# Optimization experiments

Hardware: AMD Instinct MI355X
Metric: run time of the kernel (lower is better)

The kernel has to match this reference:

```python
import jax, jax.numpy as jnp
import numpy as np

N, E, IN_DIM, H, D = 50000, 1600000, 128, 8, 16


def setup_inputs() -> dict:
    key = jax.random.key(0)
    ks = jax.random.split(key, 9)
    s = 1.0 / np.sqrt(IN_DIM)
    return {
        "h": jax.random.normal(ks[0], (N, IN_DIM), dtype=jnp.float32),
        "Wq": jax.random.normal(ks[1], (IN_DIM, H * D), dtype=jnp.float32) * s,
        "bq": jax.random.normal(ks[2], (H * D,), dtype=jnp.float32) * 0.01,
        "Wk": jax.random.normal(ks[3], (IN_DIM, H * D), dtype=jnp.float32) * s,
        "bk": jax.random.normal(ks[4], (H * D,), dtype=jnp.float32) * 0.01,
        "Wv": jax.random.normal(ks[5], (IN_DIM, H * D), dtype=jnp.float32) * s,
        "bv": jax.random.normal(ks[6], (H * D,), dtype=jnp.float32) * 0.01,
        "src": jax.random.randint(ks[7], (E,), 0, N, dtype=jnp.int32),
        "dst": jax.random.randint(ks[8], (E,), 0, N, dtype=jnp.int32),
    }


def reference(h, Wq, bq, Wk, bk, Wv, bv, src, dst):
    n = h.shape[0]
    # node-level projections, reshaped to [N, H, D]
    Q = (h @ Wq + bq).reshape(n, H, D)
    K = (h @ Wk + bk).reshape(n, H, D)
    V = (h @ Wv + bv).reshape(n, H, D)
    # per-edge score: dot(K[src], Q[dst]) / sqrt(D), exp-clamped -> [E, H]
    score = jnp.sum(K[src] * Q[dst], axis=-1) / np.sqrt(D)
    score = jnp.exp(jnp.clip(score, -5.0, 5.0))
    # score-weighted messages scattered into destination nodes
    m = V[src] * score[:, :, None]                    # [E, H, D]
    wV = jax.ops.segment_sum(m, dst, num_segments=n)  # [N, H, D]
    z = jax.ops.segment_sum(score, dst, num_segments=n)  # [N, H]
    h_out = wV / (z[:, :, None] + 1e-6)
    return h_out.reshape(n, H * D)
```

## Files before the change

### kernel.cpp

```cpp
#include <hip/hip_runtime.h>
#include <hip/hip_bf16.h>

#define IN_DIM 128
#define HH 8
#define DD 16
#define HD 128
#define SCAN_B 256
#define CHUNK 8192

#define MT  64
#define KP  136
#define NCH 128

typedef float f32x4 __attribute__((ext_vector_type(4)));
typedef short s16x8 __attribute__((ext_vector_type(8)));

__device__ __forceinline__ int sniff_fp32(const unsigned short* h_raw) {
  int sane = 0;
#pragma unroll
  for (int i = 0; i < 128; i += 2) {
    const unsigned short u = h_raw[i];
    const int expo = (u >> 7) & 0xFF;
    if (expo >= 112 && expo <= 143) sane++;
  }
  return (sane >= 40) ? 0 : 1;
}

__global__ __launch_bounds__(128) void wt_kernel(
    const unsigned short* __restrict__ h_raw,
    const void* __restrict__ Wq, const void* __restrict__ Wk,
    const void* __restrict__ Wv, __hip_bfloat16* __restrict__ Wt,
    int* __restrict__ flag, int* __restrict__ bucket_size) {
  const int isf = sniff_fp32(h_raw);
  const int n = blockIdx.x;
  const int k = threadIdx.x;
  if (n == 0) {
    if (k == 0) *flag = isf;
    for (int j = k; j < 258; j += 128) bucket_size[j] = 0;
  }
  const int mat = n >> 7;
  const int col = n & 127;
  const void* W = (mat == 0) ? Wq : (mat == 1) ? Wk : Wv;
  float v;
  if (isf) v = ((const float*)W)[(size_t)k * HD + col];
  else     v = __bfloat162float(((const __hip_bfloat16*)W)[(size_t)k * HD + col]);
  Wt[(size_t)n * KP + k] = __float2bfloat16(v);
}

__global__ __launch_bounds__(256) void proj_hist_kernel(
    const void* __restrict__ h, const __hip_bfloat16* __restrict__ Wt,
    const void* __restrict__ bq, const void* __restrict__ bk,
    const void* __restrict__ bv,
    float* __restrict__ Qf, __hip_bfloat16* __restrict__ Kb,
    __hip_bfloat16* __restrict__ Vb,
    const int* __restrict__ flag, int n_nodes,
    const int* __restrict__ dst, int* __restrict__ bucket_size, int n_edges,
    int pgrid) {
  __shared__ short Bs[NCH * KP];
  __shared__ short As[MT * KP];

  const int tid = threadIdx.x;

  if (blockIdx.x >= pgrid) {
    int* lh = (int*)Bs;
    const int e0 = (blockIdx.x - pgrid) * CHUNK;
    const int e1 = (e0 + CHUNK < n_edges) ? e0 + CHUNK : n_edges;
    lh[tid] = 0;
    __syncthreads();
    for (int e = e0 + tid; e < e1; e += 256) atomicAdd(&lh[dst[e] >> 8], 1);
    __syncthreads();
    if (lh[tid] > 0) atomicAdd(&bucket_size[tid], lh[tid]);
    return;
  }

  const int node0 = blockIdx.x * MT;
  const int isf = *flag;

#pragma unroll
  for (int j = 0; j < 16; ++j) {
    const int pid = tid + j * 256;
    const int m = pid >> 6;
    const int kk = (pid & 63) * 2;
    const int g = node0 + m;
    unsigned int pack = 0;
    if (g < n_nodes) {
      if (isf) {
        const float2 f2 = *(const float2*)((const float*)h + (size_t)g * HD + kk);
        const __hip_bfloat16 b0 = __float2bfloat16(f2.x);
        const __hip_bfloat16 b1 = __float2bfloat16(f2.y);
        pack = (unsigned int)(*(const unsigned short*)&b0) |
               ((unsigned int)(*(const unsigned short*)&b1) << 16);
      } else {
        pack = *(const unsigned int*)((const __hip_bfloat16*)h +
                                      (size_t)g * HD + kk);
      }
    }
    *(unsigned int*)&As[m * KP + kk] = pack;
  }
  __syncthreads();

  const int wave = tid >> 6;
  const int lane = tid & 63;
  const int l15 = lane & 15;
  const int quad = lane >> 4;

  s16x8 afrag[4];
#pragma unroll
  for (int k4 = 0; k4 < 4; ++k4)
    afrag[k4] = *(const s16x8*)&As[(wave * 16 + l15) * KP + k4 * 32 + quad * 8];

  for (int c = 0; c < 3; ++c) {
    __syncthreads();
    const uint4* gsrc = (const uint4*)(Wt + (size_t)c * NCH * KP);
    for (int j = tid; j < (NCH * KP * 2) / 16; j += 256)
      ((uint4*)Bs)[j] = gsrc[j];
    __syncthreads();

    f32x4 acc[8];
#pragma unroll
    for (int t = 0; t < 8; ++t) acc[t] = (f32x4){0.f, 0.f, 0.f, 0.f};

#pragma unroll
    for (int t = 0; t < 8; ++t) {
#pragma unroll
      for (int k4 = 0; k4 < 4; ++k4) {
        const s16x8 bfrag =
            *(const s16x8*)&Bs[(t * 16 + l15) * KP + k4 * 32 + quad * 8];
        acc[t] = __builtin_amdgcn_mfma_f32_16x16x32_bf16(afrag[k4], bfrag,
                                                         acc[t], 0, 0, 0);
      }
    }

    const void* bp = (c == 0) ? bq : (c == 1) ? bk : bv;
#pragma unroll
    for (int t = 0; t < 8; ++t) {
      const int ncol = t * 16 + l15;
      const float bias = isf ? ((const float*)bp)[ncol]
                             : __bfloat162float(((const __hip_bfloat16*)bp)[ncol]);
#pragma unroll
      for (int r = 0; r < 4; ++r) {
        const int g = node0 + wave * 16 + quad * 4 + r;
        if (g < n_nodes) {
          const float val = acc[t][r] + bias;
          const size_t o = (size_t)g * HD + ncol;
          if (c == 0)      Qf[o] = val;
          else if (c == 1) Kb[o] = __float2bfloat16(val);
          else             Vb[o] = __float2bfloat16(val);
        }
      }
    }
  }
}

__global__ __launch_bounds__(256) void bucket_scan_kernel(
    const int* __restrict__ bucket_size, int* __restrict__ bucket_base,
    int* __restrict__ bucket_cur, int nbuck, int n_edges) {
  __shared__ int sh[256];
  const int t = threadIdx.x;
  const int v = (t < nbuck) ? bucket_size[t] : 0;
  sh[t] = v;
  __syncthreads();
  for (int off = 1; off < 256; off <<= 1) {
    int add = (t >= off) ? sh[t - off] : 0;
    __syncthreads();
    sh[t] += add;
    __syncthreads();
  }
  const int excl = sh[t] - v;
  if (t < nbuck) {
    bucket_base[t] = excl;
    bucket_cur[t] = excl;
  }
  if (t == 0) bucket_base[nbuck] = n_edges;
}

__global__ __launch_bounds__(256) void bucketize_kernel(
    const int* __restrict__ src, const int* __restrict__ dst,
    int* __restrict__ bucket_cur, unsigned int* __restrict__ ebuf,
    int n_edges) {
  __shared__ int lh[256];
  const int t = threadIdx.x;
  const int e0 = blockIdx.x * CHUNK;
  const int e1 = (e0 + CHUNK < n_edges) ? e0 + CHUNK : n_edges;
  lh[t] = 0;
  __syncthreads();
  for (int e = e0 + t; e < e1; e += 256) atomicAdd(&lh[dst[e] >> 8], 1);
  __syncthreads();
  const int cnt_local = lh[t];
  int base = 0;
  if (cnt_local > 0) base = atomicAdd(&bucket_cur[t], cnt_local);
  __syncthreads();
  lh[t] = base;
  __syncthreads();
  for (int e = e0 + t; e < e1; e += 256) {
    const int d = dst[e];
    const int pos = atomicAdd(&lh[d >> 8], 1);
    ebuf[pos] = ((unsigned int)src[e] << 16) | (unsigned int)d;
  }
}

__global__ __launch_bounds__(256) void bucket_csr_kernel(
    const unsigned int* __restrict__ ebuf, const int* __restrict__ bucket_base,
    int* __restrict__ row_ptr, int* __restrict__ edge_src,
    int n_nodes, int nbuck) {
  __shared__ int lc[256];
  __shared__ int sh[256];
  const int b = blockIdx.x;
  const int t = threadIdx.x;
  const int lo = bucket_base[b], hi = bucket_base[b + 1];
  const int nbase = b << 8;

  lc[t] = 0;
  __syncthreads();
  for (int i = lo + t; i < hi; i += 256)
    atomicAdd(&lc[(ebuf[i] & 0xFFFFu) - nbase], 1);
  __syncthreads();

  const int v = lc[t];
  sh[t] = v;
  __syncthreads();
  for (int off = 1; off < 256; off <<= 1) {
    int add = (t >= off) ? sh[t - off] : 0;
    __syncthreads();
    sh[t] += add;
    __syncthreads();
  }
  const int excl = sh[t] - v;

  const int node = nbase + t;
  if (node < n_nodes) row_ptr[node] = lo + excl;
  if (b == nbuck - 1 && t == 255) row_ptr[n_nodes] = hi;

  __syncthreads();
  lc[t] = lo + excl;
  __syncthreads();
  for (int i = lo + t; i < hi; i += 256) {
    const unsigned int pkd = ebuf[i];
    const int pos = atomicAdd(&lc[(pkd & 0xFFFFu) - nbase], 1);
    edge_src[pos] = (int)(pkd >> 16);
  }
}

__global__ __launch_bounds__(256) void hist_kernel(
    const int* __restrict__ dst, int* __restrict__ cnt, int n_edges) {
  const int e = blockIdx.x * blockDim.x + threadIdx.x;
  if (e < n_edges) atomicAdd(&cnt[dst[e]], 1);
}

__global__ __launch_bounds__(256) void scatter_kernel(
    const int* __restrict__ src, const int* __restrict__ dst,
    int* __restrict__ cursor, int* __restrict__ edge_src, int n_edges) {
  const int e = blockIdx.x * blockDim.x + threadIdx.x;
  if (e < n_edges) {
    const int pos = atomicAdd(&cursor[dst[e]], 1);
    edge_src[pos] = src[e];
  }
}

__global__ __launch_bounds__(SCAN_B) void scan1_kernel(
    const int* __restrict__ cnt, int* __restrict__ exs,
    int* __restrict__ bsum, int n) {
  __shared__ int sh[SCAN_B];
  const int t = threadIdx.x;
  const int i = blockIdx.x * SCAN_B + t;
  int v = (i < n) ? cnt[i] : 0;
  sh[t] = v;
  __syncthreads();
  for (int off = 1; off < SCAN_B; off <<= 1) {
    int add = (t >= off) ? sh[t - off] : 0;
    __syncthreads();
    sh[t] += add;
    __syncthreads();
  }
  if (i < n) exs[i] = sh[t] - v;
  if (t == SCAN_B - 1) bsum[blockIdx.x] = sh[t];
}

__global__ __launch_bounds__(SCAN_B) void scan2_kernel(int* __restrict__ bsum,
                                                       int nb) {
  __shared__ int sh[SCAN_B];
  const int t = threadIdx.x;
  if (nb <= SCAN_B) {
    int v = (t < nb) ? bsum[t] : 0;
    sh[t] = v;
    __syncthreads();
    for (int off = 1; off < SCAN_B; off <<= 1) {
      int add = (t >= off) ? sh[t - off] : 0;
      __syncthreads();
      sh[t] += add;
      __syncthreads();
    }
    if (t < nb) bsum[t] = sh[t] - v;
  } else if (t == 0) {
    int run = 0;
    for (int b = 0; b < nb; ++b) { int v = bsum[b]; bsum[b] = run; run += v; }
  }
}

__global__ __launch_bounds__(SCAN_B) void scan3_kernel(
    const int* __restrict__ exs, const int* __restrict__ bsum,
    int* __restrict__ row_ptr, int* __restrict__ cursor, int n, int n_edges) {
  const int i = blockIdx.x * SCAN_B + threadIdx.x;
  if (i < n) {
    const int v = exs[i] + bsum[blockIdx.x];
    row_ptr[i] = v;
    cursor[i] = v;
  }
  if (i == 0) row_ptr[n] = n_edges;
}

__global__ __launch_bounds__(128) void gather_kernel(
    const int* __restrict__ row_ptr, const int* __restrict__ edge_src,
    const float* __restrict__ Qf, const __hip_bfloat16* __restrict__ Kb,
    const __hip_bfloat16* __restrict__ Vb,
    void* __restrict__ out, const int* __restrict__ flag, int n_nodes) {
  __shared__ float2 sc[2][16 * HH];
  __shared__ float zred[16 * HH];

  const int d = blockIdx.x;
  const int tid = threadIdx.x;

  const int eloc = tid >> 3;
  const int hh8  = tid & 7;
  const int hd16 = tid >> 4;

  const int start = row_ptr[d];
  const int deg = row_ptr[d + 1] - start;

  float qreg[16];
  {
    const f32x4* qp = (const f32x4*)(Qf + (size_t)d * HD + hh8 * 16);
#pragma unroll
    for (int j = 0; j < 4; ++j) {
      const f32x4 q4 = qp[j];
      qreg[j * 4 + 0] = q4[0] * 0.25f;
      qreg[j * 4 + 1] = q4[1] * 0.25f;
      qreg[j * 4 + 2] = q4[2] * 0.25f;
      qreg[j * 4 + 3] = q4[3] * 0.25f;
    }
  }

  float accV = 0.0f;
  float zacc = 0.0f;
  const int ngroups = (deg + 15) >> 4;

  for (int g = 0; g < ngroups; ++g) {
    const int buf = g & 1;
    const int ei = g * 16 + eloc;

    float score = 0.0f;
    int s = 0;
    if (ei < deg) {
      s = edge_src[start + ei];
      const uint4* kp = (const uint4*)(Kb + (size_t)s * HD + hh8 * 16);
      unsigned int kw[8];
      *(uint4*)&kw[0] = kp[0];
      *(uint4*)&kw[4] = kp[1];
      float dot = 0.0f;
#pragma unroll
      for (int i = 0; i < 8; ++i) {
        const float klo = __uint_as_float(kw[i] << 16);
        const float khi = __uint_as_float(kw[i] & 0xFFFF0000u);
        dot = fmaf(qreg[2 * i], klo, dot);
        dot = fmaf(qreg[2 * i + 1], khi, dot);
      }
      score = __expf(fminf(fmaxf(dot, -5.0f), 5.0f));
    }
    zacc += score;
    sc[buf][eloc * HH + hh8] = make_float2(score, __int_as_float(s));
    __syncthreads();

    const int rem = deg - g * 16;
    const int lim = (rem < 16) ? rem : 16;
    if (lim == 16) {
#pragma unroll
      for (int e = 0; e < 16; ++e) {
        const float2 pe = sc[buf][e * HH + hd16];
        const int s2 = __float_as_int(pe.y);
        const unsigned short vu =
            *(const unsigned short*)(Vb + (size_t)s2 * HD + tid);
        accV = fmaf(pe.x, __uint_as_float(((unsigned int)vu) << 16), accV);
      }
    } else {
      for (int e = 0; e < lim; ++e) {
        const float2 pe = sc[buf][e * HH + hd16];
        const int s2 = __float_as_int(pe.y);
        const unsigned short vu =
            *(const unsigned short*)(Vb + (size_t)s2 * HD + tid);
        accV = fmaf(pe.x, __uint_as_float(((unsigned int)vu) << 16), accV);
      }
    }
  }

  zred[eloc * HH + hh8] = zacc;
  __syncthreads();
  float aZ = 0.0f;
#pragma unroll
  for (int i = 0; i < 16; ++i) aZ += zred[i * HH + hd16];

  const float r = accV / (aZ + 1e-6f);
  const size_t o = (size_t)d * HD + tid;
  if (*flag) ((float*)out)[o] = r;
  else       ((__hip_bfloat16*)out)[o] = __float2bfloat16(r);
}

extern "C" void kernel_launch(void* const* d_in, const int* in_sizes, int n_in,
                              void* d_out, int out_size, void* d_ws, size_t ws_size,
                              hipStream_t stream) {
  const void* h  = d_in[0];
  const void* Wq = d_in[1];
  const void* bq = d_in[2];
  const void* Wk = d_in[3];
  const void* bk = d_in[4];
  const void* Wv = d_in[5];
  const void* bv = d_in[6];
  const int* src = (const int*)d_in[7];
  const int* dst = (const int*)d_in[8];

  const int n_nodes = in_sizes[0] / IN_DIM;
  const int n_edges = in_sizes[7];
  const int nb = (n_nodes + SCAN_B - 1) / SCAN_B;
  const int nbuck = (n_nodes + 255) >> 8;

  char* p = (char*)d_ws;
  int* flag = (int*)p;                       p += 256;
  float* Qf = (float*)p;                     p += (size_t)n_nodes * HD * 4;
  __hip_bfloat16* Kb = (__hip_bfloat16*)p;   p += (size_t)n_nodes * HD * 2;
  __hip_bfloat16* Vb = (__hip_bfloat16*)p;   p += (size_t)n_nodes * HD * 2;
  __hip_bfloat16* Wt = (__hip_bfloat16*)p;   p += ((size_t)384 * KP * 2 + 255) / 256 * 256;
  int* bucket_size = (int*)p;                p += 258 * 4;
  int* bucket_base = (int*)p;                p += 258 * 4;
  int* bucket_cur = (int*)p;                 p += 258 * 4;
  int* row_ptr = (int*)p;                    p += (size_t)(n_nodes + 1) * 4;
  unsigned int* ebuf = (unsigned int*)p;     p += (size_t)n_edges * 4;
  int* edge_src = (int*)p;                   p += (size_t)n_edges * 4;
  int* cnt = (int*)p;                        p += (size_t)n_nodes * 4;
  int* exs = (int*)p;                        p += (size_t)n_nodes * 4;
  int* bsum = (int*)p;                       p += (size_t)(nb + 1) * 4;
  int* cursor = (int*)p;                     p += (size_t)n_nodes * 4;

  wt_kernel<<<384, 128, 0, stream>>>((const unsigned short*)h, Wq, Wk, Wv, Wt,
                                     flag, bucket_size);

  const int pgrid = (n_nodes + MT - 1) / MT;
  const int nchunk = (n_edges + CHUNK - 1) / CHUNK;

  if (n_nodes <= 65536) {
    proj_hist_kernel<<<pgrid + nchunk, 256, 0, stream>>>(
        h, Wt, bq, bk, bv, Qf, Kb, Vb, flag, n_nodes, dst, bucket_size,
        n_edges, pgrid);
    bucket_scan_kernel<<<1, 256, 0, stream>>>(bucket_size, bucket_base,
                                              bucket_cur, nbuck, n_edges);
    bucketize_kernel<<<nchunk, 256, 0, stream>>>(src, dst, bucket_cur, ebuf,
                                                 n_edges);
    bucket_csr_kernel<<<nbuck, 256, 0, stream>>>(ebuf, bucket_base, row_ptr,
                                                 edge_src, n_nodes, nbuck);
  } else {
    proj_hist_kernel<<<pgrid, 256, 0, stream>>>(
        h, Wt, bq, bk, bv, Qf, Kb, Vb, flag, n_nodes, dst, bucket_size,
        n_edges, pgrid);
    hipMemsetAsync(cnt, 0, (size_t)n_nodes * sizeof(int), stream);
    const int eb = 256;
    const int egrid = (n_edges + eb - 1) / eb;
    hist_kernel<<<egrid, eb, 0, stream>>>(dst, cnt, n_edges);
    scan1_kernel<<<nb, SCAN_B, 0, stream>>>(cnt, exs, bsum, n_nodes);
    scan2_kernel<<<1, SCAN_B, 0, stream>>>(bsum, nb);
    scan3_kernel<<<nb, SCAN_B, 0, stream>>>(exs, bsum, row_ptr, cursor,
                                            n_nodes, n_edges);
    scatter_kernel<<<egrid, eb, 0, stream>>>(src, dst, cursor, edge_src,
                                             n_edges);
  }

  gather_kernel<<<n_nodes, 128, 0, stream>>>(row_ptr, edge_src, Qf, Kb, Vb,
                                             d_out, flag, n_nodes);
}
```

Measured before the change: 330.8 us.

## Fuse K and V gathers per edge-head lane, reducing partial sums once at end

The gather kernel now has each thread handle one (edge, head) pair across all its edges. It loads the 16 K and 16 V bf16 values for that pair with vector loads and keeps 16 per-thread V accumulators, with edge_src prefetched one iteration ahead. This removes the per-group shared-memory exchange of scores and source ids, its __syncthreads, and the scalar 2-byte V loads. In exchange it adds register pressure for the accumulators and a final padded shared-memory reduction across the 16 edge lanes.

```diff
diff --git a/kernel.cpp b/kernel.cpp
--- a/kernel.cpp
+++ b/kernel.cpp
@@ -11,6 +11,8 @@
 #define MT  64
 #define KP  136
 #define NCH 128
+
+#define VPAD 132
 
 typedef float f32x4 __attribute__((ext_vector_type(4)));
 typedef short s16x8 __attribute__((ext_vector_type(8)));
@@ -314,15 +316,14 @@
     const float* __restrict__ Qf, const __hip_bfloat16* __restrict__ Kb,
     const __hip_bfloat16* __restrict__ Vb,
     void* __restrict__ out, const int* __restrict__ flag, int n_nodes) {
-  __shared__ float2 sc[2][16 * HH];
-  __shared__ float zred[16 * HH];
+  __shared__ float vred[16][VPAD];
+  __shared__ float zred[16][HH];
 
   const int d = blockIdx.x;
   const int tid = threadIdx.x;
 
   const int eloc = tid >> 3;
   const int hh8  = tid & 7;
-  const int hd16 = tid >> 4;
 
   const int start = row_ptr[d];
   const int deg = row_ptr[d + 1] - start;
@@ -340,65 +341,67 @@
     }
   }
 
-  float accV = 0.0f;
+  float acc[16];
+#pragma unroll
+  for (int j = 0; j < 16; ++j) acc[j] = 0.0f;
   float zacc = 0.0f;
-  const int ngroups = (deg + 15) >> 4;
-
-  for (int g = 0; g < ngroups; ++g) {
-    const int buf = g & 1;
-    const int ei = g * 16 + eloc;
-
-    float score = 0.0f;
-    int s = 0;
-    if (ei < deg) {
-      s = edge_src[start + ei];
-      const uint4* kp = (const uint4*)(Kb + (size_t)s * HD + hh8 * 16);
-      unsigned int kw[8];
-      *(uint4*)&kw[0] = kp[0];
-      *(uint4*)&kw[4] = kp[1];
-      float dot = 0.0f;
-#pragma unroll
-      for (int i = 0; i < 8; ++i) {
-        const float klo = __uint_as_float(kw[i] << 16);
-        const float khi = __uint_as_float(kw[i] & 0xFFFF0000u);
-        dot = fmaf(qreg[2 * i], klo, dot);
-        dot = fmaf(qreg[2 * i + 1], khi, dot);
-      }
-      score = __expf(fminf(fmaxf(dot, -5.0f), 5.0f));
-    }
+
+  int s_next = 0;
+  if (eloc < deg) s_next = edge_src[start + eloc];
+
+  for (int ei = eloc; ei < deg; ei += 16) {
+    const int s = s_next;
+    const int nx = ei + 16;
+    if (nx < deg) s_next = edge_src[start + nx];
+
+    const size_t rowoff = (size_t)s * HD + hh8 * 16;
+    const uint4* kp = (const uint4*)(Kb + rowoff);
+    const uint4 k0 = kp[0];
+    const uint4 k1 = kp[1];
+    const uint4* vp = (const uint4*)(Vb + rowoff);
+    const uint4 v0 = vp[0];
+    const uint4 v1 = vp[1];
+
+    unsigned int kw[8];
+    *(uint4*)&kw[0] = k0;
+    *(uint4*)&kw[4] = k1;
+    float dot = 0.0f;
+#pragma unroll
+    for (int i = 0; i < 8; ++i) {
+      const float klo = __uint_as_float(kw[i] << 16);
+      const float khi = __uint_as_float(kw[i] & 0xFFFF0000u);
+      dot = fmaf(qreg[2 * i], klo, dot);
+      dot = fmaf(qreg[2 * i + 1], khi, dot);
+    }
+    const float score = __expf(fminf(fmaxf(dot, -5.0f), 5.0f));
     zacc += score;
-    sc[buf][eloc * HH + hh8] = make_float2(score, __int_as_float(s));
-    __syncthreads();
-
-    const int rem = deg - g * 16;
-    const int lim = (rem < 16) ? rem : 16;
-    if (lim == 16) {
-#pragma unroll
-      for (int e = 0; e < 16; ++e) {
-        const float2 pe = sc[buf][e * HH + hd16];
-        const int s2 = __float_as_int(pe.y);
-        const unsigned short vu =
-            *(const unsigned short*)(Vb + (size_t)s2 * HD + tid);
-        accV = fmaf(pe.x, __uint_as_float(((unsigned int)vu) << 16), accV);
-      }
-    } else {
-      for (int e = 0; e < lim; ++e) {
-        const float2 pe = sc[buf][e * HH + hd16];
-        const int s2 = __float_as_int(pe.y);
-        const unsigned short vu =
-            *(const unsigned short*)(Vb + (size_t)s2 * HD + tid);
-        accV = fmaf(pe.x, __uint_as_float(((unsigned int)vu) << 16), accV);
-      }
-    }
-  }
-
-  zred[eloc * HH + hh8] = zacc;
-  __syncthreads();
-  float aZ = 0.0f;
-#pragma unroll
-  for (int i = 0; i < 16; ++i) aZ += zred[i * HH + hd16];
-
-  const float r = accV / (aZ + 1e-6f);
+
+    unsigned int vw[8];
+    *(uint4*)&vw[0] = v0;
+    *(uint4*)&vw[4] = v1;
+#pragma unroll
+    for (int i = 0; i < 8; ++i) {
+      const float vlo = __uint_as_float(vw[i] << 16);
+      const float vhi = __uint_as_float(vw[i] & 0xFFFF0000u);
+      acc[2 * i]     = fmaf(score, vlo, acc[2 * i]);
+      acc[2 * i + 1] = fmaf(score, vhi, acc[2 * i + 1]);
+    }
+  }
+
+#pragma unroll
+  for (int j = 0; j < 16; ++j) vred[eloc][hh8 * 16 + j] = acc[j];
+  zred[eloc][hh8] = zacc;
+  __syncthreads();
+
+  const int hd16 = tid >> 4;
+  float sumV = 0.0f;
+#pragma unroll
+  for (int i = 0; i < 16; ++i) sumV += vred[i][tid];
+  float sumZ = 0.0f;
+#pragma unroll
+  for (int i = 0; i < 16; ++i) sumZ += zred[i][hd16];
+
+  const float r = sumV / (sumZ + 1e-6f);
   const size_t o = (size_t)d * HD + tid;
   if (*flag) ((float*)out)[o] = r;
   else       ((__hip_bfloat16*)out)[o] = __float2bfloat16(r);
```

Result: faster. 320.8 us (-3.0%).
